# Optimization experiments

Measured on AMD Instinct MI355X. Metric: run time of the kernel, lower is better.

Reference implementation:

```python
import jax, jax.numpy as jnp
import numpy as np

B, K, N, D = 2048, 32, 50000, 128


def setup_inputs() -> dict:
    key = jax.random.key(0)
    k1, k2 = jax.random.split(key)
    embed = jax.random.normal(k1, (N, D), dtype=jnp.float32)
    neigh_idx = jax.random.randint(k2, (B, K), 0, N, dtype=jnp.int32)
    return {"embed": embed, "neigh_idx": neigh_idx}


def reference(embed, neigh_idx):
    # embed: [N, D] feature table (the `features` lookup materialized)
    # neigh_idx: [B, K] sampled neighbor node ids per batch node
    b, k = neigh_idx.shape
    n = embed.shape[0]
    rows = jnp.repeat(jnp.arange(b, dtype=jnp.int32), k)           # [B*K]
    cols = neigh_idx.reshape(-1)                                    # [B*K]
    # dense 0/1 mask, duplicates collapse to 1 (set semantics in original)
    mask = jnp.zeros((b, n), dtype=embed.dtype).at[rows, cols].set(1.0)
    num_neigh = mask.sum(axis=1, keepdims=True)                     # [B, 1]
    mask = mask / num_neigh                                         # row-normalized
    to_feats = mask @ embed                                         # [B, D] mean of neighbor feats
    return to_feats
```

## Files before the change

kernel.cpp:

```cpp
#include <hip/hip_runtime.h>
#include <hip/hip_bf16.h>


#define KNEIGH 32
#define DIM 128

__global__ __launch_bounds__(64) void mean_agg_kernel(
    const float* __restrict__ embed,
    const int* __restrict__ neigh_idx,
    float* __restrict__ out)
{
    const int b    = blockIdx.x;
    const int t    = threadIdx.x;
    const int slot = t & 31;
    const int g    = t >> 5;

    const int v = neigh_idx[b * KNEIGH + slot];

    int dup = 0;
    #pragma unroll
    for (int j = 0; j < KNEIGH - 1; ++j) {
        const int vj = __shfl(v, j);
        dup |= (j < slot) & (vj == v);
    }
    const float w   = dup ? 0.0f : 1.0f;
    const int   off = v * DIM;

    const unsigned long long m = __ballot(!dup);
    const float inv = 1.0f / (float)__popcll(m & 0xffffffffull);

    float4 acc = make_float4(0.f, 0.f, 0.f, 0.f);
    #pragma unroll
    for (int k = 0; k < KNEIGH / 2; ++k) {
        const int   r    = 2 * k + g;
        const float wr   = __shfl(w, r);
        const int   offr = __shfl(off, r);
        const float4 val = *reinterpret_cast<const float4*>(
            embed + offr + (slot << 2));
        acc.x = fmaf(wr, val.x, acc.x);
        acc.y = fmaf(wr, val.y, acc.y);
        acc.z = fmaf(wr, val.z, acc.z);
        acc.w = fmaf(wr, val.w, acc.w);
    }

    acc.x += __shfl_xor(acc.x, 32);
    acc.y += __shfl_xor(acc.y, 32);
    acc.z += __shfl_xor(acc.z, 32);
    acc.w += __shfl_xor(acc.w, 32);

    if (t < 32) {
        float4 r;
        r.x = acc.x * inv;
        r.y = acc.y * inv;
        r.z = acc.z * inv;
        r.w = acc.w * inv;
        *reinterpret_cast<float4*>(out + b * DIM + (slot << 2)) = r;
    }
}

extern "C" void kernel_launch(void* const* d_in, const int* in_sizes, int n_in,
                              void* d_out, int out_size, void* d_ws, size_t ws_size,
                              hipStream_t stream) {
    const float* embed     = (const float*)d_in[0];
    const int*   neigh_idx = (const int*)d_in[1];
    float*       out       = (float*)d_out;

    const int B = in_sizes[1] / KNEIGH;

    mean_agg_kernel<<<B, 64, 0, stream>>>(embed, neigh_idx, out);
}
```

Before: 69.90 us.

## Spread neighbor gather across four waves per batch row with LDS reduction

Each block grows from one wave to four (256 threads). One wave deduplicates the neighbor ids and writes offsets and weights to shared memory, then all 8 half-wave groups each gather 4 neighbor rows. Partial sums are reduced through shared memory. The aim is more memory-level parallelism per row and shorter per-thread load chains; the cost is two block barriers and extra LDS traffic.

```diff
diff --git a/kernel.cpp b/kernel.cpp
--- a/kernel.cpp
+++ b/kernel.cpp
@@ -5,42 +5,49 @@
 #define KNEIGH 32
 #define DIM 128
 
-__global__ __launch_bounds__(64) void mean_agg_kernel(
+__global__ __launch_bounds__(256) void mean_agg_kernel(
     const float* __restrict__ embed,
     const int* __restrict__ neigh_idx,
     float* __restrict__ out)
 {
-    const int b    = blockIdx.x;
-    const int t    = threadIdx.x;
-    const int slot = t & 31;
-    const int g    = t >> 5;
+    __shared__ int    s_off[KNEIGH];
+    __shared__ float  s_w[KNEIGH];
+    __shared__ float  s_inv;
+    __shared__ float4 s_part[3][32];
 
-    const int v = neigh_idx[b * KNEIGH + slot];
+    const int b = blockIdx.x;
+    const int t = threadIdx.x;
 
-    int dup = 0;
-    #pragma unroll
-    for (int j = 0; j < KNEIGH - 1; ++j) {
-        const int vj = __shfl(v, j);
-        dup |= (j < slot) & (vj == v);
+    if (t < KNEIGH) {
+        const int v = neigh_idx[b * KNEIGH + t];
+        int dup = 0;
+        #pragma unroll
+        for (int j = 0; j < KNEIGH - 1; ++j) {
+            const int vj = __shfl(v, j);
+            dup |= (j < t) & (vj == v);
+        }
+        s_off[t] = v * DIM;
+        s_w[t]   = dup ? 0.0f : 1.0f;
+        const unsigned long long m = __ballot(!dup);
+        if (t == 0) s_inv = 1.0f / (float)__popcll(m & 0xffffffffull);
     }
-    const float w   = dup ? 0.0f : 1.0f;
-    const int   off = v * DIM;
+    __syncthreads();
 
-    const unsigned long long m = __ballot(!dup);
-    const float inv = 1.0f / (float)__popcll(m & 0xffffffffull);
+    const int chunk = t & 31;
+    const int g     = t >> 5;
 
     float4 acc = make_float4(0.f, 0.f, 0.f, 0.f);
     #pragma unroll
-    for (int k = 0; k < KNEIGH / 2; ++k) {
-        const int   r    = 2 * k + g;
-        const float wr   = __shfl(w, r);
-        const int   offr = __shfl(off, r);
-        const float4 val = *reinterpret_cast<const float4*>(
-            embed + offr + (slot << 2));
-        acc.x = fmaf(wr, val.x, acc.x);
-        acc.y = fmaf(wr, val.y, acc.y);
-        acc.z = fmaf(wr, val.z, acc.z);
-        acc.w = fmaf(wr, val.w, acc.w);
+    for (int k = 0; k < 4; ++k) {
+        const int   r   = 8 * k + g;
+        const float w   = s_w[r];
+        const int   off = s_off[r];
+        const float4 v  = *reinterpret_cast<const float4*>(
+            embed + off + (chunk << 2));
+        acc.x = fmaf(w, v.x, acc.x);
+        acc.y = fmaf(w, v.y, acc.y);
+        acc.z = fmaf(w, v.z, acc.z);
+        acc.w = fmaf(w, v.w, acc.w);
     }
 
     acc.x += __shfl_xor(acc.x, 32);
@@ -48,13 +55,23 @@
     acc.z += __shfl_xor(acc.z, 32);
     acc.w += __shfl_xor(acc.w, 32);
 
+    const int wv = t >> 6;
+    if (wv > 0 && (t & 63) < 32) {
+        s_part[wv - 1][chunk] = acc;
+    }
+    __syncthreads();
+
     if (t < 32) {
+        const float4 p0 = s_part[0][t];
+        const float4 p1 = s_part[1][t];
+        const float4 p2 = s_part[2][t];
+        const float  inv = s_inv;
         float4 r;
-        r.x = acc.x * inv;
-        r.y = acc.y * inv;
-        r.z = acc.z * inv;
-        r.w = acc.w * inv;
-        *reinterpret_cast<float4*>(out + b * DIM + (slot << 2)) = r;
+        r.x = ((acc.x + p0.x) + (p1.x + p2.x)) * inv;
+        r.y = ((acc.y + p0.y) + (p1.y + p2.y)) * inv;
+        r.z = ((acc.z + p0.z) + (p1.z + p2.z)) * inv;
+        r.w = ((acc.w + p0.w) + (p1.w + p2.w)) * inv;
+        *reinterpret_cast<float4*>(out + b * DIM + (t << 2)) = r;
     }
 }
 
@@ -67,5 +84,5 @@
 
     const int B = in_sizes[1] / KNEIGH;
 
-    mean_agg_kernel<<<B, 64, 0, stream>>>(embed, neigh_idx, out);
+    mean_agg_kernel<<<B, 256, 0, stream>>>(embed, neigh_idx, out);
 }
```

Result: no change. 71.28 us (+2.0%).
